# Optimization experiments

Hardware: AMD Instinct MI355X
Metric: run time of the kernel (lower is better)

Reference implementation:

```python
import jax, jax.numpy as jnp
import numpy as np

EPS = 1e-12  # torch F.normalize eps


def _l2_normalize(x):
    # F.normalize(x, p=2, dim=-1): x / max(||x||_2, eps)
    norm = jnp.sqrt(jnp.sum(x * x, axis=-1, keepdims=True))
    return x / jnp.maximum(norm, EPS)


def setup_inputs() -> dict:
    key = jax.random.key(0)
    kq, kk, kv = jax.random.split(key, 3)
    shape = (4, 4096, 1024)  # [batch, seq, embed_size]
    return {
        "q": jax.random.normal(kq, shape, dtype=jnp.float32),
        "k": jax.random.normal(kk, shape, dtype=jnp.float32),
        "v": jax.random.normal(kv, shape, dtype=jnp.float32),
    }


def reference(q, k, v):
    # Note: the module's nn.Linear layers are unused in its forward; q,k,v
    # are consumed directly. reduce=True path (default).
    Q = _l2_normalize(q)
    K = _l2_normalize(k)
    # attention_scores = Q @ K^T : [b, n, n] (no softmax)
    attention_weights = jnp.einsum("bnd,bmd->bnm", Q, K)
    # attention_outputs = scores @ V : [b, n, d]
    attention_outputs = jnp.einsum("bnm,bmd->bnd", attention_weights, v)
    return attention_outputs, attention_weights
```

## Files before the change

### kernel.cpp

```cpp
#include <hip/hip_runtime.h>


#define SEQ 4096
#define EMB 1024
#define NBATCH 4

typedef __attribute__((ext_vector_type(8))) __bf16 bf16x8;
typedef __attribute__((ext_vector_type(4))) float f32x4;
typedef const __attribute__((address_space(1))) void* gas_ptr;
typedef __attribute__((address_space(3))) void* las_ptr;

__device__ __forceinline__ void gld_lds16(const void* g, void* l) {
    __builtin_amdgcn_global_load_lds((gas_ptr)g, (las_ptr)l, 16, 0, 0);
}

__device__ __forceinline__ unsigned short f2bf(float f) {
    unsigned int u = __builtin_bit_cast(unsigned int, f);
    u += 0x7FFFu + ((u >> 16) & 1u);
    return (unsigned short)(u >> 16);
}

__device__ __forceinline__ bf16x8 ld_bf16x8(const unsigned short* p) {
    int4 v = *(const int4*)p;
    return __builtin_bit_cast(bf16x8, v);
}

__global__ __launch_bounds__(256) void norm_rows_kernel(const float* __restrict__ src,
                                                        unsigned short* __restrict__ dst) {
    int row = blockIdx.x;
    int t = threadIdx.x;
    float4 v = *(const float4*)(src + (size_t)row * EMB + t * 4);
    float ss = v.x * v.x + v.y * v.y + v.z * v.z + v.w * v.w;
#pragma unroll
    for (int off = 32; off > 0; off >>= 1) ss += __shfl_down(ss, off, 64);
    __shared__ float red[4];
    if ((t & 63) == 0) red[t >> 6] = ss;
    __syncthreads();
    float tot = red[0] + red[1] + red[2] + red[3];
    float scale = 1.0f / fmaxf(sqrtf(tot), 1e-12f);
    ushort4 o;
    o.x = f2bf(v.x * scale);
    o.y = f2bf(v.y * scale);
    o.z = f2bf(v.z * scale);
    o.w = f2bf(v.w * scale);
    *(ushort4*)(dst + (size_t)row * EMB + t * 4) = o;
}

__global__ __launch_bounds__(256) void transpose_v_kernel(const float* __restrict__ v,
                                                          unsigned short* __restrict__ vt) {
    __shared__ __align__(16) unsigned short T[64][68];
    int b = blockIdx.z;
    int j0 = blockIdx.x * 64;
    int d0 = blockIdx.y * 64;
    const float* vb = v + (size_t)b * SEQ * EMB;
    unsigned short* vtb = vt + (size_t)b * (size_t)EMB * SEQ;
    int t = threadIdx.x;
#pragma unroll
    for (int i = 0; i < 4; i++) {
        int lin = t + i * 256;
        int j = lin >> 4;
        int dseg = lin & 15;
        float4 x = *(const float4*)(vb + (size_t)(j0 + j) * EMB + d0 + dseg * 4);
        ushort4 o;
        o.x = f2bf(x.x); o.y = f2bf(x.y); o.z = f2bf(x.z); o.w = f2bf(x.w);
        *(ushort4*)&T[j][dseg * 4] = o;
    }
    __syncthreads();
#pragma unroll
    for (int i = 0; i < 4; i++) {
        int lin = t + i * 256;
        int d = lin >> 4;
        int jseg = lin & 15;
        ushort4 o;
        o.x = T[jseg * 4 + 0][d];
        o.y = T[jseg * 4 + 1][d];
        o.z = T[jseg * 4 + 2][d];
        o.w = T[jseg * 4 + 3][d];
        *(ushort4*)(vtb + (size_t)(d0 + d) * SEQ + j0 + jseg * 4) = o;
    }
}

template <int AMODE, bool WBF16>
__global__ __launch_bounds__(256) void gemm_tile_kernel(
    const void* __restrict__ Av, const unsigned short* __restrict__ B,
    float* __restrict__ C, unsigned short* __restrict__ Cb16,
    int lda, int ldb, int ldc, int K,
    long long strideA, long long strideB, long long strideC) {
    __shared__ __align__(16) unsigned short As[128][32];
    __shared__ __align__(16) unsigned short Bs[128][32];

    int b = blockIdx.z;
    int m0 = blockIdx.y * 128;
    int n0 = blockIdx.x * 128;
    const unsigned short* Ab = nullptr;
    const float* Af = nullptr;
    if constexpr (AMODE == 1)
        Af = (const float*)Av + (size_t)b * strideA;
    else
        Ab = (const unsigned short*)Av + (size_t)b * strideA;
    const unsigned short* Bb = B + (size_t)b * strideB;
    float* Cb = C + (size_t)b * strideC;
    unsigned short* Cb16b = WBF16 ? Cb16 + (size_t)b * strideC : nullptr;

    int tid = threadIdx.x;
    int wave = tid >> 6, lane = tid & 63;
    int wr = wave >> 1, wc = wave & 1;
    int quad = lane >> 4, l16 = lane & 15;

    f32x4 acc[4][4] = {};

    for (int k0 = 0; k0 < K; k0 += 32) {
        __syncthreads();
        if constexpr (AMODE == 0) {
#pragma unroll
            for (int i = 0; i < 2; i++) {
                int c = tid + i * 256;
                int row = c >> 2, seg = c & 3;
                gld_lds16(Ab + (size_t)(m0 + row) * lda + k0 + seg * 8,
                          (unsigned short*)As + c * 8);
            }
        } else {
#pragma unroll
            for (int i = 0; i < 4; i++) {
                int lin = tid + i * 256;
                int row = lin >> 3;
                int seg = lin & 7;
                float4 x = *(const float4*)(Af + (size_t)(m0 + row) * lda + k0 + seg * 4);
                ushort4 o;
                o.x = f2bf(x.x); o.y = f2bf(x.y); o.z = f2bf(x.z); o.w = f2bf(x.w);
                *(ushort4*)&As[row][seg * 4] = o;
            }
        }
#pragma unroll
        for (int i = 0; i < 2; i++) {
            int c = tid + i * 256;
            int row = c >> 2, seg = c & 3;
            gld_lds16(Bb + (size_t)(n0 + row) * ldb + k0 + seg * 8,
                      (unsigned short*)Bs + c * 8);
        }
        __syncthreads();

        bf16x8 afr[4], bfr[4];
#pragma unroll
        for (int mt = 0; mt < 4; mt++)
            afr[mt] = ld_bf16x8(&As[wr * 64 + mt * 16 + l16][quad * 8]);
#pragma unroll
        for (int nt = 0; nt < 4; nt++)
            bfr[nt] = ld_bf16x8(&Bs[wc * 64 + nt * 16 + l16][quad * 8]);
#pragma unroll
        for (int mt = 0; mt < 4; mt++)
#pragma unroll
            for (int nt = 0; nt < 4; nt++)
                acc[mt][nt] = __builtin_amdgcn_mfma_f32_16x16x32_bf16(
                    afr[mt], bfr[nt], acc[mt][nt], 0, 0, 0);
    }

#pragma unroll
    for (int mt = 0; mt < 4; mt++) {
#pragma unroll
        for (int nt = 0; nt < 4; nt++) {
            int row = m0 + wr * 64 + mt * 16 + quad * 4;
            int col = n0 + wc * 64 + nt * 16 + l16;
#pragma unroll
            for (int r = 0; r < 4; r++) {
                float val = acc[mt][nt][r];
                Cb[(size_t)(row + r) * ldc + col] = val;
                if constexpr (WBF16)
                    Cb16b[(size_t)(row + r) * ldc + col] = f2bf(val);
            }
        }
    }
}

extern "C" void kernel_launch(void* const* d_in, const int* in_sizes, int n_in,
                              void* d_out, int out_size, void* d_ws, size_t ws_size,
                              hipStream_t stream) {
    const float* q = (const float*)d_in[0];
    const float* k = (const float*)d_in[1];
    const float* v = (const float*)d_in[2];

    const size_t elems = (size_t)NBATCH * SEQ * EMB;
    const size_t welems = (size_t)NBATCH * SEQ * SEQ;
    unsigned short* Qn = (unsigned short*)d_ws;
    unsigned short* Kn = Qn + elems;
    unsigned short* Vt = Kn + elems;
    unsigned short* Wb = Vt + elems;
    const size_t ws_needed = (3 * elems + welems) * sizeof(unsigned short);
    const bool fast = ws_size >= ws_needed;

    float* O = (float*)d_out;
    float* W = O + elems;

    norm_rows_kernel<<<NBATCH * SEQ, 256, 0, stream>>>(q, Qn);
    norm_rows_kernel<<<NBATCH * SEQ, 256, 0, stream>>>(k, Kn);
    transpose_v_kernel<<<dim3(SEQ / 64, EMB / 64, NBATCH), 256, 0, stream>>>(v, Vt);

    if (fast) {
        gemm_tile_kernel<0, true><<<dim3(SEQ / 128, SEQ / 128, NBATCH), 256, 0, stream>>>(
            Qn, Kn, W, Wb, EMB, EMB, SEQ, EMB,
            (long long)SEQ * EMB, (long long)SEQ * EMB, (long long)SEQ * SEQ);
        gemm_tile_kernel<0, false><<<dim3(EMB / 128, SEQ / 128, NBATCH), 256, 0, stream>>>(
            Wb, Vt, O, nullptr, SEQ, SEQ, EMB, SEQ,
            (long long)SEQ * SEQ, (long long)EMB * SEQ, (long long)SEQ * EMB);
    } else {
        gemm_tile_kernel<0, false><<<dim3(SEQ / 128, SEQ / 128, NBATCH), 256, 0, stream>>>(
            Qn, Kn, W, nullptr, EMB, EMB, SEQ, EMB,
            (long long)SEQ * EMB, (long long)SEQ * EMB, (long long)SEQ * SEQ);
        gemm_tile_kernel<1, false><<<dim3(EMB / 128, SEQ / 128, NBATCH), 256, 0, stream>>>(
            W, Vt, O, nullptr, SEQ, SEQ, EMB, SEQ,
            (long long)SEQ * SEQ, (long long)EMB * SEQ, (long long)SEQ * EMB);
    }
}
```

Baseline: 871.5 us.

## Replace GEMM tiles with 256x256 double-buffered, swizzled, pipelined MFMA kernel

Adds a new GEMM kernel for the fast path. It uses 256x256 output tiles, 512 threads, K-steps of 64, double-buffered LDS filled by global_load_lds, and an XOR swizzle to avoid bank conflicts. Loads for the next K tile are interleaved with MFMA groups using manual waitcnt, barriers and setprio, aiming to hide memory latency and raise data reuse over the old 128x128 single-buffer kernel. In exchange it needs 128KB of LDS and many accumulator registers per thread, and the hand-written vmcnt and barrier scheduling is fragile.

```diff
diff --git a/kernel.cpp b/kernel.cpp
--- a/kernel.cpp
+++ b/kernel.cpp
@@ -80,14 +80,162 @@
     }
 }
 
+
+#define BAR __builtin_amdgcn_s_barrier()
+#define LGKM0 asm volatile("s_waitcnt lgkmcnt(0)" ::: "memory")
+#define VMCNT4 asm volatile("s_waitcnt vmcnt(4)" ::: "memory")
+#define VMCNT0 asm volatile("s_waitcnt vmcnt(0)" ::: "memory")
+
+#define MFMA1(MI, NI, AF, BV) \
+    acc[MI][NI] = __builtin_amdgcn_mfma_f32_16x16x32_bf16(AF, BV, acc[MI][NI], 0, 0, 0)
+
+#define MFMA16(MH, NH, BF) do { \
+    __builtin_amdgcn_s_setprio(1); \
+    MFMA1((MH)*4+0, (NH)*2+0, af[0][0], BF[0][0]); \
+    MFMA1((MH)*4+0, (NH)*2+1, af[0][0], BF[1][0]); \
+    MFMA1((MH)*4+1, (NH)*2+0, af[1][0], BF[0][0]); \
+    MFMA1((MH)*4+1, (NH)*2+1, af[1][0], BF[1][0]); \
+    MFMA1((MH)*4+2, (NH)*2+0, af[2][0], BF[0][0]); \
+    MFMA1((MH)*4+2, (NH)*2+1, af[2][0], BF[1][0]); \
+    MFMA1((MH)*4+3, (NH)*2+0, af[3][0], BF[0][0]); \
+    MFMA1((MH)*4+3, (NH)*2+1, af[3][0], BF[1][0]); \
+    MFMA1((MH)*4+0, (NH)*2+0, af[0][1], BF[0][1]); \
+    MFMA1((MH)*4+0, (NH)*2+1, af[0][1], BF[1][1]); \
+    MFMA1((MH)*4+1, (NH)*2+0, af[1][1], BF[0][1]); \
+    MFMA1((MH)*4+1, (NH)*2+1, af[1][1], BF[1][1]); \
+    MFMA1((MH)*4+2, (NH)*2+0, af[2][1], BF[0][1]); \
+    MFMA1((MH)*4+2, (NH)*2+1, af[2][1], BF[1][1]); \
+    MFMA1((MH)*4+3, (NH)*2+0, af[3][1], BF[0][1]); \
+    MFMA1((MH)*4+3, (NH)*2+1, af[3][1], BF[1][1]); \
+    __builtin_amdgcn_s_setprio(0); \
+} while (0)
+
+#define LD_A(BUF, MH) do { \
+    const unsigned short (*Ac)[64] = As[BUF]; \
+    int rb = (MH) * 128 + wr * 64 + l16; \
+    af[0][0] = ld_bf16x8(&Ac[rb +  0][swz0]); af[0][1] = ld_bf16x8(&Ac[rb +  0][swz1]); \
+    af[1][0] = ld_bf16x8(&Ac[rb + 16][swz0]); af[1][1] = ld_bf16x8(&Ac[rb + 16][swz1]); \
+    af[2][0] = ld_bf16x8(&Ac[rb + 32][swz0]); af[2][1] = ld_bf16x8(&Ac[rb + 32][swz1]); \
+    af[3][0] = ld_bf16x8(&Ac[rb + 48][swz0]); af[3][1] = ld_bf16x8(&Ac[rb + 48][swz1]); \
+} while (0)
+
+#define LD_B(BUF, NH, BF) do { \
+    const unsigned short (*Bc)[64] = Bs[BUF]; \
+    int rb = (NH) * 128 + wc * 32 + l16; \
+    BF[0][0] = ld_bf16x8(&Bc[rb +  0][swz0]); BF[0][1] = ld_bf16x8(&Bc[rb +  0][swz1]); \
+    BF[1][0] = ld_bf16x8(&Bc[rb + 16][swz0]); BF[1][1] = ld_bf16x8(&Bc[rb + 16][swz1]); \
+} while (0)
+
+#define STAGE_A(NB, AH, KN) do { \
+    gld_lds16(Ab + (AH) * aHalf + ro0 + (KN), (unsigned short*)As[NB] + (AH) * 8192 + lc0); \
+    gld_lds16(Ab + (AH) * aHalf + ro1 + (KN), (unsigned short*)As[NB] + (AH) * 8192 + lc1); \
+} while (0)
+
+#define STAGE_B(NB, BH, KN) do { \
+    gld_lds16(Bb + (BH) * bHalf + sb0 + (KN), (unsigned short*)Bs[NB] + (BH) * 8192 + lc0); \
+    gld_lds16(Bb + (BH) * bHalf + sb1 + (KN), (unsigned short*)Bs[NB] + (BH) * 8192 + lc1); \
+} while (0)
+
+#define KTILE(CB, NB, KN, DOSTAGE) do { \
+     \
+    LD_A(CB, 0); LD_B(CB, 0, b0); \
+    if (DOSTAGE) STAGE_A(NB, 0, KN); \
+    BAR; LGKM0; \
+    MFMA16(0, 0, b0); \
+    VMCNT4; BAR; \
+     \
+    LD_B(CB, 1, b1); \
+    if (DOSTAGE) STAGE_B(NB, 0, KN); \
+    BAR; LGKM0; \
+    MFMA16(0, 1, b1); \
+    VMCNT4; BAR; \
+     \
+    LD_A(CB, 1); \
+    if (DOSTAGE) STAGE_B(NB, 1, KN); \
+    BAR; LGKM0; \
+    MFMA16(1, 1, b1); \
+    BAR; \
+     \
+    if (DOSTAGE) STAGE_A(NB, 1, KN); \
+    BAR; LGKM0; \
+    MFMA16(1, 0, b0); \
+    VMCNT4; BAR; \
+} while (0)
+
+template <bool WBF16>
+__global__ __launch_bounds__(512, 2) void gemm256_kernel(
+    const unsigned short* __restrict__ A, const unsigned short* __restrict__ B,
+    float* __restrict__ C, unsigned short* __restrict__ Cb16,
+    int lda, int ldb, int ldc, int K,
+    long long strideA, long long strideB, long long strideC) {
+    __shared__ __align__(16) unsigned short As[2][256][64];
+    __shared__ __align__(16) unsigned short Bs[2][256][64];
+
+    int bz = blockIdx.z;
+    int m0 = blockIdx.y * 256;
+    int n0 = blockIdx.x * 256;
+    const unsigned short* Ab = A + (size_t)bz * strideA + (size_t)m0 * lda;
+    const unsigned short* Bb = B + (size_t)bz * strideB + (size_t)n0 * ldb;
+    float* Cb = C + (size_t)bz * strideC;
+    unsigned short* Cb16b = WBF16 ? Cb16 + (size_t)bz * strideC : nullptr;
+
+    int tid = threadIdx.x;
+    int wave = tid >> 6, lane = tid & 63;
+    int wr = wave >> 2, wc = wave & 3;
+    int quad = lane >> 4, l16 = lane & 15;
+    int swz0 = ((quad) ^ (l16 & 7)) * 8;
+    int swz1 = ((quad + 4) ^ (l16 & 7)) * 8;
+
+    int r0 = tid >> 3;
+    int cs0 = ((tid & 7) ^ (r0 & 7)) * 8;
+    const int aHalf = 128 * lda, bHalf = 128 * ldb;
+    int ro0 = r0 * lda + cs0;
+    int ro1 = (r0 + 64) * lda + cs0;
+    int sb0 = r0 * ldb + cs0;
+    int sb1 = (r0 + 64) * ldb + cs0;
+    unsigned lc0 = (unsigned)(tid * 8);
+    unsigned lc1 = (unsigned)(tid * 8 + 4096);
+
+    f32x4 acc[8][4] = {};
+    bf16x8 af[4][2], b0[2][2], b1[2][2];
+
+    const int NT = K >> 6;
+
+    STAGE_A(0, 0, 0); STAGE_B(0, 0, 0); STAGE_B(0, 1, 0); STAGE_A(0, 1, 0);
+    VMCNT4; BAR;
+
+    for (int i = 0; i < (NT >> 1) - 1; ++i) {
+        KTILE(0, 1, ((2 * i + 1) << 6), 1);
+        KTILE(1, 0, ((2 * i + 2) << 6), 1);
+    }
+    KTILE(0, 1, ((NT - 1) << 6), 1);
+    VMCNT0; BAR;
+    KTILE(1, 0, 0, 0);
+
+#pragma unroll
+    for (int mt8 = 0; mt8 < 8; ++mt8) {
+        int row = m0 + (mt8 >> 2) * 128 + wr * 64 + (mt8 & 3) * 16 + quad * 4;
+#pragma unroll
+        for (int nt4 = 0; nt4 < 4; ++nt4) {
+            int col = n0 + (nt4 >> 1) * 128 + wc * 32 + (nt4 & 1) * 16 + l16;
+#pragma unroll
+            for (int r = 0; r < 4; ++r) {
+                float val = acc[mt8][nt4][r];
+                Cb[(size_t)(row + r) * ldc + col] = val;
+                if (WBF16) Cb16b[(size_t)(row + r) * ldc + col] = f2bf(val);
+            }
+        }
+    }
+}
+
 template <int AMODE, bool WBF16>
 __global__ __launch_bounds__(256) void gemm_tile_kernel(
     const void* __restrict__ Av, const unsigned short* __restrict__ B,
     float* __restrict__ C, unsigned short* __restrict__ Cb16,
     int lda, int ldb, int ldc, int K,
     long long strideA, long long strideB, long long strideC) {
-    __shared__ __align__(16) unsigned short As[128][32];
-    __shared__ __align__(16) unsigned short Bs[128][32];
+    __shared__ __align__(16) unsigned short Asl[128][32];
+    __shared__ __align__(16) unsigned short Bsl[128][32];
 
     int b = blockIdx.z;
     int m0 = blockIdx.y * 128;
@@ -117,7 +265,7 @@
                 int c = tid + i * 256;
                 int row = c >> 2, seg = c & 3;
                 gld_lds16(Ab + (size_t)(m0 + row) * lda + k0 + seg * 8,
-                          (unsigned short*)As + c * 8);
+                          (unsigned short*)Asl + c * 8);
             }
         } else {
 #pragma unroll
@@ -128,7 +276,7 @@
                 float4 x = *(const float4*)(Af + (size_t)(m0 + row) * lda + k0 + seg * 4);
                 ushort4 o;
                 o.x = f2bf(x.x); o.y = f2bf(x.y); o.z = f2bf(x.z); o.w = f2bf(x.w);
-                *(ushort4*)&As[row][seg * 4] = o;
+                *(ushort4*)&Asl[row][seg * 4] = o;
             }
         }
 #pragma unroll
@@ -136,17 +284,17 @@
             int c = tid + i * 256;
             int row = c >> 2, seg = c & 3;
             gld_lds16(Bb + (size_t)(n0 + row) * ldb + k0 + seg * 8,
-                      (unsigned short*)Bs + c * 8);
+                      (unsigned short*)Bsl + c * 8);
         }
         __syncthreads();
 
         bf16x8 afr[4], bfr[4];
 #pragma unroll
         for (int mt = 0; mt < 4; mt++)
-            afr[mt] = ld_bf16x8(&As[wr * 64 + mt * 16 + l16][quad * 8]);
+            afr[mt] = ld_bf16x8(&Asl[wr * 64 + mt * 16 + l16][quad * 8]);
 #pragma unroll
         for (int nt = 0; nt < 4; nt++)
-            bfr[nt] = ld_bf16x8(&Bs[wc * 64 + nt * 16 + l16][quad * 8]);
+            bfr[nt] = ld_bf16x8(&Bsl[wc * 64 + nt * 16 + l16][quad * 8]);
 #pragma unroll
         for (int mt = 0; mt < 4; mt++)
 #pragma unroll
@@ -196,10 +344,10 @@
     transpose_v_kernel<<<dim3(SEQ / 64, EMB / 64, NBATCH), 256, 0, stream>>>(v, Vt);
 
     if (fast) {
-        gemm_tile_kernel<0, true><<<dim3(SEQ / 128, SEQ / 128, NBATCH), 256, 0, stream>>>(
+        gemm256_kernel<true><<<dim3(SEQ / 256, SEQ / 256, NBATCH), 512, 0, stream>>>(
             Qn, Kn, W, Wb, EMB, EMB, SEQ, EMB,
             (long long)SEQ * EMB, (long long)SEQ * EMB, (long long)SEQ * SEQ);
-        gemm_tile_kernel<0, false><<<dim3(EMB / 128, SEQ / 128, NBATCH), 256, 0, stream>>>(
+        gemm256_kernel<false><<<dim3(EMB / 256, SEQ / 256, NBATCH), 512, 0, stream>>>(
             Wb, Vt, O, nullptr, SEQ, SEQ, EMB, SEQ,
             (long long)SEQ * SEQ, (long long)EMB * SEQ, (long long)SEQ * EMB);
     } else {
```

Result: faster. 738.8 us (-15.2%).
